# Optimization experiments

Hardware: AMD Instinct MI355X
Metric: run time of the kernel (lower is better)

The kernel has to match this reference:

```python
import jax, jax.numpy as jnp
import numpy as np

B, N, E = 2, 2048, 2048
H, G, D = 16, 4, 128          # num_heads, num_kv_groups, head_dim = E // H
HID = 4 * E                    # GeGLU hidden width
EPS = 1e-6


def setup_inputs() -> dict:
    key = jax.random.key(0)
    ks = jax.random.split(key, 8)
    g = lambda k, shape: jax.random.normal(k, shape, jnp.float32) * 0.02
    return {
        "x": jax.random.normal(ks[0], (B, N, E), jnp.float32),
        "wq": g(ks[1], (E, H * D)),
        "wk": g(ks[2], (E, G * D)),
        "wv": g(ks[3], (E, G * D)),
        "wo": g(ks[4], (H * D, E)),
        "w1": g(ks[5], (E, 2 * HID)),   # GeGLU in-proj (value | gate)
        "w2": g(ks[6], (HID, E)),       # GeGLU out-proj
        "norm1_w": jnp.ones((E,), jnp.float32),
        "norm2_w": jnp.ones((E,), jnp.float32),
    }


def _rope_cos_sin(n, d, dtype):
    inv_freq = 1.0 / (10000.0 ** (jnp.arange(0, d, 2, dtype=jnp.float32) / d))
    freqs = jnp.arange(n, dtype=jnp.float32)[:, None] * inv_freq[None, :]  # [n, d/2]
    emb = jnp.concatenate([freqs, freqs], axis=-1)                          # [n, d]
    return jnp.cos(emb).astype(dtype), jnp.sin(emb).astype(dtype)


def _rotate_half(t):
    d2 = t.shape[-1] // 2
    return jnp.concatenate([-t[..., d2:], t[..., :d2]], axis=-1)


def _apply_rope(t, cos, sin):
    # t: [b, h, n, d]; cos/sin: [n, d]
    return t * cos + _rotate_half(t) * sin


def _rmsnorm(x, w):
    var = jnp.mean(jnp.square(x), axis=-1, keepdims=True)
    return x * jax.lax.rsqrt(var + EPS) * w


def reference(x, wq, wk, wv, wo, w1, w2, norm1_w, norm2_w):
    b, n, _ = x.shape
    # q = k = v = x reshaped into heads (pre-projection, as in source)
    qkv = x.reshape(b, n, H, D).transpose(0, 2, 1, 3)  # [b, H, n, D]
    cos, sin = _rope_cos_sin(n, D, x.dtype)
    q_r = _apply_rope(qkv, cos, sin)
    k_r = _apply_rope(qkv, cos, sin)
    # flatten back to [b, n, E]
    q_flat = q_r.transpose(0, 2, 1, 3).reshape(b, n, E)
    k_flat = k_r.transpose(0, 2, 1, 3).reshape(b, n, E)
    v_flat = x  # v untouched by RoPE; flatten == x

    # Grouped-query attention with internal projections
    qh = (q_flat @ wq).reshape(b, n, H, D).transpose(0, 2, 1, 3)       # [b, H, n, D]
    kh = (k_flat @ wk).reshape(b, n, G, D)                              # [b, n, G, D]
    vh = (v_flat @ wv).reshape(b, n, G, D)
    kh = jnp.repeat(kh, H // G, axis=2).transpose(0, 2, 1, 3)           # [b, H, n, D]
    vh = jnp.repeat(vh, H // G, axis=2).transpose(0, 2, 1, 3)

    scale = 1.0 / np.sqrt(D)
    scores = jnp.einsum('bhqd,bhkd->bhqk', qh, kh) * scale
    attn = jax.nn.softmax(scores, axis=-1)                               # [b, H, n, n]
    ctx = jnp.einsum('bhqk,bhkd->bhqd', attn, vh)
    attn_out = ctx.transpose(0, 2, 1, 3).reshape(b, n, H * D) @ wo      # [b, n, E]

    x1 = _rmsnorm(x + attn_out, norm1_w)

    # GeGLU FFN
    uv = x1 @ w1
    u, gate = jnp.split(uv, 2, axis=-1)
    fc = (u * jax.nn.gelu(gate)) @ w2

    x2 = _rmsnorm(x1 + fc, norm2_w)
    return (x2, (k_flat, v_flat), attn)
```

## Files before the change

### kernel.cpp

```cpp
#include <hip/hip_runtime.h>
#include <hip/hip_bf16.h>


using f32x4  = __attribute__((ext_vector_type(4))) float;
using bf16x8 = __attribute__((ext_vector_type(8))) short;
using bf16x4 = __attribute__((ext_vector_type(4))) short;
using u16x4  = __attribute__((ext_vector_type(4))) unsigned short;

#define DEV __device__ __forceinline__

#define ASYNC16(lds, g)                                                        \
  __builtin_amdgcn_global_load_lds(                                           \
      (const __attribute__((address_space(1))) void*)(g),                      \
      (__attribute__((address_space(3))) void*)(lds), 16, 0, 0)

DEV unsigned short f2bf(float f) {
  unsigned int u = __float_as_uint(f);
  return (unsigned short)((u + 0x7fffu + ((u >> 16) & 1u)) >> 16);
}
DEV float bf2f(unsigned short h) {
  return __uint_as_float(((unsigned int)h) << 16);
}

DEV float waveRedSum(float v) {
#pragma unroll
  for (int o = 32; o; o >>= 1) v += __shfl_xor(v, o);
  return v;
}

__global__ __launch_bounds__(256) void kconvT(const float* __restrict__ in,
                                              unsigned short* __restrict__ out,
                                              int K, int N) {
  __shared__ float tile[32][33];
  int bx = blockIdx.x * 32;
  int by = blockIdx.y * 32;
  int tx = threadIdx.x & 31;
  int ty = threadIdx.x >> 5;
#pragma unroll
  for (int i = 0; i < 32; i += 8)
    tile[ty + i][tx] = in[(size_t)(by + ty + i) * N + bx + tx];
  __syncthreads();
#pragma unroll
  for (int i = 0; i < 32; i += 8)
    out[(size_t)(bx + ty + i) * K + by + tx] = f2bf(tile[tx][ty + i]);
}

__global__ __launch_bounds__(256) void krope(const float* __restrict__ x,
                                             float* __restrict__ kout,
                                             float* __restrict__ vout,
                                             unsigned short* __restrict__ xq,
                                             unsigned short* __restrict__ xb) {
  int idx = blockIdx.x * 256 + threadIdx.x;
  int f  = idx & 63;
  int h  = (idx >> 6) & 15;
  int bn = idx >> 10;
  int n  = bn & 2047;
  size_t base = (size_t)bn * 2048 + h * 128;
  float inv = exp2f((float)f * (-13.287712379549449f / 64.0f));
  float ang = (float)n * inv;
  float c = cosf(ang), s = sinf(ang);
  float a = x[base + f], b = x[base + f + 64];
  float k1 = a * c - b * s;
  float k2 = b * c + a * s;
  __builtin_nontemporal_store(k1, kout + base + f);
  __builtin_nontemporal_store(k2, kout + base + f + 64);
  xq[base + f]      = f2bf(k1);
  xq[base + f + 64] = f2bf(k2);
  __builtin_nontemporal_store(a, vout + base + f);
  __builtin_nontemporal_store(b, vout + base + f + 64);
  xb[base + f]      = f2bf(a);
  xb[base + f + 64] = f2bf(b);
}

__global__ __launch_bounds__(256) void krms1(const float* __restrict__ x,
                                             const float* __restrict__ ao,
                                             const float* __restrict__ w,
                                             unsigned short* __restrict__ x1b) {
  size_t row = blockIdx.x;
  const f32x4* xp = (const f32x4*)(x + row * 2048);
  const f32x4* ap = (const f32x4*)(ao + row * 2048);
  int tid = threadIdx.x;
  f32x4 t0 = xp[tid * 2] + ap[tid * 2];
  f32x4 t1 = xp[tid * 2 + 1] + ap[tid * 2 + 1];
  float ss = 0.f;
#pragma unroll
  for (int i = 0; i < 4; ++i) ss += t0[i] * t0[i] + t1[i] * t1[i];
  ss = waveRedSum(ss);
  __shared__ float red[4];
  int wid = tid >> 6, lane = tid & 63;
  if (!lane) red[wid] = ss;
  __syncthreads();
  ss = red[0] + red[1] + red[2] + red[3];
  float rr = rsqrtf(ss * (1.0f / 2048.0f) + 1e-6f);
  const f32x4* wp = (const f32x4*)w;
  f32x4 w0 = wp[tid * 2], w1 = wp[tid * 2 + 1];
  u16x4 o0, o1;
#pragma unroll
  for (int i = 0; i < 4; ++i) {
    o0[i] = f2bf(t0[i] * rr * w0[i]);
    o1[i] = f2bf(t1[i] * rr * w1[i]);
  }
  u16x4* op = (u16x4*)(x1b + row * 2048);
  op[tid * 2] = o0;
  op[tid * 2 + 1] = o1;
}

__global__ __launch_bounds__(256) void krms2(const unsigned short* __restrict__ x1b,
                                             const unsigned short* __restrict__ fc,
                                             const float* __restrict__ w,
                                             float* __restrict__ out) {
  size_t row = blockIdx.x;
  const u16x4* xp = (const u16x4*)(x1b + row * 2048);
  const u16x4* fp = (const u16x4*)(fc + row * 2048);
  int tid = threadIdx.x;
  u16x4 a0 = xp[tid * 2], a1 = xp[tid * 2 + 1];
  u16x4 b0 = fp[tid * 2], b1 = fp[tid * 2 + 1];
  f32x4 t0, t1;
#pragma unroll
  for (int i = 0; i < 4; ++i) {
    t0[i] = bf2f(a0[i]) + bf2f(b0[i]);
    t1[i] = bf2f(a1[i]) + bf2f(b1[i]);
  }
  float ss = 0.f;
#pragma unroll
  for (int i = 0; i < 4; ++i) ss += t0[i] * t0[i] + t1[i] * t1[i];
  ss = waveRedSum(ss);
  __shared__ float red[4];
  int wid = tid >> 6, lane = tid & 63;
  if (!lane) red[wid] = ss;
  __syncthreads();
  ss = red[0] + red[1] + red[2] + red[3];
  float rr = rsqrtf(ss * (1.0f / 2048.0f) + 1e-6f);
  const f32x4* wp = (const f32x4*)w;
  f32x4 w0 = wp[tid * 2], w1 = wp[tid * 2 + 1];
  f32x4* op = (f32x4*)(out + row * 2048);
  f32x4 o0 = t0 * rr * w0;
  f32x4 o1 = t1 * rr * w1;
  __builtin_nontemporal_store(o0, op + tid * 2);
  __builtin_nontemporal_store(o1, op + tid * 2 + 1);
}

template <bool OUT_BF16, bool TRANS_OUT>
__global__ __launch_bounds__(256, 2) void gemm_bt(
    const unsigned short* __restrict__ A, const unsigned short* __restrict__ Bt,
    void* __restrict__ C_, int K, int lda, int ldb, int ldc, float alpha) {
  __shared__ unsigned short As[128 * 32];
  __shared__ unsigned short Bs[128 * 32];
  const int tid = threadIdx.x;
  const int bm0 = blockIdx.y * 128, bn0 = blockIdx.x * 128;

  f32x4 acc[4][4] = {};

  const int lane = tid & 63, wid = tid >> 6;
  const int wr = wid >> 1, wc = wid & 1;
  const int lr = lane & 15, kq = lane >> 4;
  const int srow = tid >> 2;
  const int scol = (tid & 3) * 8;
  unsigned short* AsW = As + tid * 8;
  unsigned short* BsW = Bs + tid * 8;

  for (int kt = 0; kt < K; kt += 32) {
    ASYNC16(AsW,        A + (size_t)(bm0 + srow)      * lda + kt + scol);
    ASYNC16(AsW + 2048, A + (size_t)(bm0 + srow + 64) * lda + kt + scol);
    ASYNC16(BsW,        Bt + (size_t)(bn0 + srow)      * ldb + kt + scol);
    ASYNC16(BsW + 2048, Bt + (size_t)(bn0 + srow + 64) * ldb + kt + scol);
    __syncthreads();
    bf16x8 afr[4], bfr[4];
#pragma unroll
    for (int i = 0; i < 4; ++i)
      afr[i] = *(const bf16x8*)&As[(wr * 64 + i * 16 + lr) * 32 + kq * 8];
#pragma unroll
    for (int j = 0; j < 4; ++j)
      bfr[j] = *(const bf16x8*)&Bs[(wc * 64 + j * 16 + lr) * 32 + kq * 8];
#pragma unroll
    for (int i = 0; i < 4; ++i)
#pragma unroll
      for (int j = 0; j < 4; ++j)
        acc[i][j] = __builtin_amdgcn_mfma_f32_16x16x32_bf16(afr[i], bfr[j],
                                                            acc[i][j], 0, 0, 0);
    __syncthreads();
  }

#pragma unroll
  for (int i = 0; i < 4; ++i)
#pragma unroll
    for (int j = 0; j < 4; ++j) {
      int rowb = bm0 + wr * 64 + i * 16 + kq * 4;
      int col = bn0 + wc * 64 + j * 16 + lr;
#pragma unroll
      for (int r = 0; r < 4; ++r) {
        float v = acc[i][j][r] * alpha;
        size_t idx = TRANS_OUT ? ((size_t)col * ldc + (rowb + r))
                               : ((size_t)(rowb + r) * ldc + col);
        if constexpr (OUT_BF16)
          ((unsigned short*)C_)[idx] = f2bf(v);
        else
          ((float*)C_)[idx] = v;
      }
    }
}

__global__ __launch_bounds__(512, 4) void kattn(
    const unsigned short* __restrict__ qh,
    const unsigned short* __restrict__ kh,
    const unsigned short* __restrict__ vT,
    float* __restrict__ attn,
    unsigned short* __restrict__ ctx) {
  __shared__ __align__(16) char U[65536];
  __shared__ __align__(16) char Vb[16384];
  float* redm = (float*)Vb;
  float* reds = redm + 128;

  const int tid = threadIdx.x;
  const int lane = tid & 63, w = tid >> 6;
  const int lr = lane & 15, kq = lane >> 4;
  const int bid = blockIdx.x;
  const int g8 = bid & 7;
  const int j  = bid >> 3;
  const int bz = g8 >> 2;
  const int gz = g8 & 3;
  const int hz = gz * 4 + (j & 3);
  const int q0 = (j >> 2) << 4;
  const int z  = bz * 16 + hz;

  const unsigned short* Aq =
      qh + ((size_t)(bz * 2048 + q0 + lr) * 2048 + hz * 128);
  bf16x8 qfr[4];
#pragma unroll
  for (int kk = 0; kk < 4; ++kk)
    qfr[kk] = *(const bf16x8*)(Aq + kk * 32 + kq * 8);

  const unsigned short* Kb =
      kh + ((size_t)(bz * 2048) * 512 + gz * 128);
  int krow[4], kcs[4];
#pragma unroll
  for (int R = 0; R < 4; ++R) {
    int idx = R * 64 + lane;
    krow[R] = idx >> 4;
    kcs[R] = (idx & 15) ^ (krow[R] & 7);
  }
  auto stageK = [&](int buf, int t) {
#pragma unroll
    for (int R = 0; R < 4; ++R)
      ASYNC16(U + buf * 32768 + w * 4096 + (R * 64 + lane) * 16,
              Kb + (size_t)(t * 128 + w * 16 + krow[R]) * 512 + kcs[R] * 8);
  };

  f32x4 acc[16];
#pragma unroll
  for (int t = 0; t < 16; ++t) acc[t] = f32x4{0.f, 0.f, 0.f, 0.f};

  stageK(0, 0);
  stageK(1, 1);
#pragma unroll
  for (int t = 0; t < 16; ++t) {
    if (t < 15) asm volatile("s_waitcnt vmcnt(4)" ::: "memory");
    else        asm volatile("s_waitcnt vmcnt(0)" ::: "memory");
    __builtin_amdgcn_sched_barrier(0);
    const char* Kw = U + (t & 1) * 32768 + w * 4096;
    bf16x8 kfr[4];
#pragma unroll
    for (int kk = 0; kk < 4; ++kk) {
      int cch = (kk * 4 + kq) ^ (lr & 7);
      kfr[kk] = *(const bf16x8*)(Kw + lr * 256 + cch * 16);
    }
    asm volatile("s_waitcnt lgkmcnt(0)" ::: "memory");
    __builtin_amdgcn_sched_barrier(0);
    if (t + 2 < 16) stageK(t & 1, t + 2);
#pragma unroll
    for (int kk = 0; kk < 4; ++kk)
      acc[t] = __builtin_amdgcn_mfma_f32_16x16x32_bf16(kfr[kk], qfr[kk],
                                                       acc[t], 0, 0, 0);
  }

  const float scale = 0.08838834764831845f;
  float mx = -3.4e38f;
#pragma unroll
  for (int t = 0; t < 16; ++t) {
    acc[t] *= scale;
#pragma unroll
    for (int r = 0; r < 4; ++r) mx = fmaxf(mx, acc[t][r]);
  }
  mx = fmaxf(mx, __shfl_xor(mx, 16));
  mx = fmaxf(mx, __shfl_xor(mx, 32));
  if (kq == 0) redm[w * 16 + lr] = mx;
  __syncthreads();
  mx = redm[lr];
#pragma unroll
  for (int ww = 1; ww < 8; ++ww) mx = fmaxf(mx, redm[ww * 16 + lr]);

  float sm = 0.f;
#pragma unroll
  for (int t = 0; t < 16; ++t) {
#pragma unroll
    for (int r = 0; r < 4; ++r) {
      float e = __expf(acc[t][r] - mx);
      acc[t][r] = e;
      sm += e;
    }
  }
  sm += __shfl_xor(sm, 16);
  sm += __shfl_xor(sm, 32);
  if (kq == 0) reds[w * 16 + lr] = sm;
  __syncthreads();
  float smt = reds[lr];
#pragma unroll
  for (int ww = 1; ww < 8; ++ww) smt += reds[ww * 16 + lr];
  float inv = 1.0f / smt;

  float* arow = attn + (((size_t)z * 2048 + q0 + lr) * 2048);
#pragma unroll
  for (int t = 0; t < 16; ++t) {
    int key = t * 128 + w * 16 + kq * 4;
    f32x4 p = acc[t] * inv;
    __builtin_nontemporal_store(p, (f32x4*)(arow + key));
    bf16x4 pb;
#pragma unroll
    for (int r = 0; r < 4; ++r) pb[r] = (short)f2bf(p[r]);
    int c8 = key >> 3;
    *(bf16x4*)(U + lr * 4096 + ((c8 ^ (lr & 7)) << 4) + ((key & 7) << 1)) = pb;
  }
  __syncthreads();

  const unsigned short* Bv = vT + (size_t)gz * 524288 + bz * 2048;
  const int d0 = w * 16;
  const int vd = lane >> 2;
  const int vcs = (lane & 3) ^ (vd & 3);
  auto stageV = [&](int buf, int t) {
    ASYNC16(Vb + buf * 8192 + w * 1024 + lane * 16,
            Bv + (size_t)(d0 + vd) * 4096 + t * 32 + vcs * 8);
  };

  f32x4 cfr = {};
  stageV(0, 0);
  stageV(1, 1);
#pragma unroll
  for (int t = 0; t < 64; ++t) {
    if (t < 63) asm volatile("s_waitcnt vmcnt(1)" ::: "memory");
    else        asm volatile("s_waitcnt vmcnt(0)" ::: "memory");
    __builtin_amdgcn_sched_barrier(0);
    int c8 = t * 4 + kq;
    bf16x8 pfr = *(const bf16x8*)(U + lr * 4096 + ((c8 ^ (lr & 7)) << 4));
    const char* Vw = Vb + (t & 1) * 8192 + w * 1024;
    bf16x8 vfr = *(const bf16x8*)(Vw + lr * 64 + ((kq ^ (lr & 3)) << 4));
    asm volatile("s_waitcnt lgkmcnt(0)" ::: "memory");
    __builtin_amdgcn_sched_barrier(0);
    if (t + 2 < 64) stageV(t & 1, t + 2);
    cfr = __builtin_amdgcn_mfma_f32_16x16x32_bf16(pfr, vfr, cfr, 0, 0, 0);
  }
#pragma unroll
  for (int r = 0; r < 4; ++r) {
    int q = kq * 4 + r;
    ctx[((size_t)(bz * 2048 + q0 + q) * 2048) + hz * 128 + d0 + lr] =
        f2bf(cfr[r]);
  }
}

template <bool OUT_BF16>
__global__ __launch_bounds__(512, 2) void gemm128(
    const unsigned short* __restrict__ A, const unsigned short* __restrict__ Bt,
    void* __restrict__ C_, int K, int lda, int ldb, int ldc) {
  __shared__ unsigned short As[2][128 * 64];
  __shared__ unsigned short Bs[2][128 * 64];
  const int tid = threadIdx.x;
  const int bm0 = blockIdx.y * 128, bn0 = blockIdx.x * 128;
  const int lane = tid & 63, wid = tid >> 6;
  const int wr = wid >> 2, wc = wid & 3;
  const int lr = lane & 15, kq = lane >> 4;

  f32x4 acc[4][2] = {};

  int sArow[2], sAcc[2];
#pragma unroll
  for (int R = 0; R < 2; ++R) {
    int c = R * 512 + tid;
    sArow[R] = c >> 3;
    sAcc[R]  = (c & 7) ^ (sArow[R] & 7);
  }

  auto stage = [&](int buf, int k0) {
#pragma unroll
    for (int R = 0; R < 2; ++R)
      ASYNC16(&As[buf][(R * 512 + tid) * 8],
              A + (size_t)(bm0 + sArow[R]) * lda + k0 + sAcc[R] * 8);
#pragma unroll
    for (int R = 0; R < 2; ++R)
      ASYNC16(&Bs[buf][(R * 512 + tid) * 8],
              Bt + (size_t)(bn0 + sArow[R]) * ldb + k0 + sAcc[R] * 8);
  };

  const int NT = K >> 6;
  stage(0, 0);
  stage(1, 64);
  int cur = 0;
  for (int t = 0; t < NT; ++t) {
    if (t + 1 < NT) asm volatile("s_waitcnt vmcnt(4)" ::: "memory");
    else            asm volatile("s_waitcnt vmcnt(0)" ::: "memory");
    __builtin_amdgcn_sched_barrier(0);
    __builtin_amdgcn_s_barrier();
    __builtin_amdgcn_sched_barrier(0);
    const unsigned short* Ac = As[cur];
    const unsigned short* Bc = Bs[cur];
    bf16x8 afr0[4], bfr0[2];
#pragma unroll
    for (int i = 0; i < 4; ++i) {
      int row = wr * 64 + i * 16 + lr;
      afr0[i] = *(const bf16x8*)&Ac[(row * 8 + (kq ^ (row & 7))) * 8];
    }
#pragma unroll
    for (int j2 = 0; j2 < 2; ++j2) {
      int brow = wc * 32 + j2 * 16 + lr;
      bfr0[j2] = *(const bf16x8*)&Bc[(brow * 8 + (kq ^ (brow & 7))) * 8];
    }
    __builtin_amdgcn_s_setprio(1);
#pragma unroll
    for (int j2 = 0; j2 < 2; ++j2)
#pragma unroll
      for (int i = 0; i < 4; ++i)
        acc[i][j2] = __builtin_amdgcn_mfma_f32_16x16x32_bf16(afr0[i], bfr0[j2],
                                                             acc[i][j2], 0, 0, 0);
    __builtin_amdgcn_s_setprio(0);
    bf16x8 afr1[4], bfr1[2];
#pragma unroll
    for (int i = 0; i < 4; ++i) {
      int row = wr * 64 + i * 16 + lr;
      afr1[i] = *(const bf16x8*)&Ac[(row * 8 + ((4 + kq) ^ (row & 7))) * 8];
    }
#pragma unroll
    for (int j2 = 0; j2 < 2; ++j2) {
      int brow = wc * 32 + j2 * 16 + lr;
      bfr1[j2] = *(const bf16x8*)&Bc[(brow * 8 + ((4 + kq) ^ (brow & 7))) * 8];
    }
    asm volatile("s_waitcnt lgkmcnt(0)" ::: "memory");
    __builtin_amdgcn_sched_barrier(0);
    __builtin_amdgcn_s_barrier();
    __builtin_amdgcn_sched_barrier(0);
    if (t + 2 < NT) stage(cur, (t + 2) << 6);
    __builtin_amdgcn_s_setprio(1);
#pragma unroll
    for (int j2 = 0; j2 < 2; ++j2)
#pragma unroll
      for (int i = 0; i < 4; ++i)
        acc[i][j2] = __builtin_amdgcn_mfma_f32_16x16x32_bf16(afr1[i], bfr1[j2],
                                                             acc[i][j2], 0, 0, 0);
    __builtin_amdgcn_s_setprio(0);
    cur ^= 1;
  }

#pragma unroll
  for (int i = 0; i < 4; ++i)
#pragma unroll
    for (int j = 0; j < 2; ++j) {
      int rowb = bm0 + wr * 64 + i * 16 + kq * 4;
      int col = bn0 + wc * 32 + j * 16 + lr;
#pragma unroll
      for (int r = 0; r < 4; ++r) {
        if constexpr (OUT_BF16)
          ((unsigned short*)C_)[(size_t)(rowb + r) * ldc + col] = f2bf(acc[i][j][r]);
        else
          ((float*)C_)[(size_t)(rowb + r) * ldc + col] = acc[i][j][r];
      }
    }
}

__global__ __launch_bounds__(512, 2) void gemm_geglu256(
    const unsigned short* __restrict__ A, const unsigned short* __restrict__ B1,
    const unsigned short* __restrict__ B2, unsigned short* __restrict__ H_,
    int K, int lda, int ldb, int ldc) {
  __shared__ unsigned short As[2][256 * 64];
  __shared__ unsigned short B1s[2][128 * 64];
  __shared__ unsigned short B2s[2][128 * 64];
  const int tid = threadIdx.x;
  const int bm0 = blockIdx.y * 256, bn0 = blockIdx.x * 128;
  const int lane = tid & 63, wid = tid >> 6;
  const int wr = wid >> 2, wc = wid & 3;
  const int lr = lane & 15, kq = lane >> 4;

  f32x4 accu[8][2] = {};
  f32x4 accg[8][2] = {};

  int sArow[4], sAcc[4], sBrow[2], sBcc[2];
#pragma unroll
  for (int R = 0; R < 4; ++R) {
    int c = R * 512 + tid;
    sArow[R] = c >> 3;
    sAcc[R]  = (c & 7) ^ (sArow[R] & 7);
  }
#pragma unroll
  for (int R = 0; R < 2; ++R) {
    int c = R * 512 + tid;
    sBrow[R] = c >> 3;
    sBcc[R]  = (c & 7) ^ (sBrow[R] & 7);
  }

  auto stage = [&](int buf, int k0) {
#pragma unroll
    for (int R = 0; R < 4; ++R)
      ASYNC16(&As[buf][(R * 512 + tid) * 8],
              A + (size_t)(bm0 + sArow[R]) * lda + k0 + sAcc[R] * 8);
#pragma unroll
    for (int R = 0; R < 2; ++R)
      ASYNC16(&B1s[buf][(R * 512 + tid) * 8],
              B1 + (size_t)(bn0 + sBrow[R]) * ldb + k0 + sBcc[R] * 8);
#pragma unroll
    for (int R = 0; R < 2; ++R)
      ASYNC16(&B2s[buf][(R * 512 + tid) * 8],
              B2 + (size_t)(bn0 + sBrow[R]) * ldb + k0 + sBcc[R] * 8);
  };

  const int NT = K >> 6;
  stage(0, 0);
  stage(1, 64);
  int cur = 0;
  for (int t = 0; t < NT; ++t) {
    if (t + 1 < NT) asm volatile("s_waitcnt vmcnt(8)" ::: "memory");
    else            asm volatile("s_waitcnt vmcnt(0)" ::: "memory");
    __builtin_amdgcn_sched_barrier(0);
    __builtin_amdgcn_s_barrier();
    __builtin_amdgcn_sched_barrier(0);
    const unsigned short* Ac = As[cur];
    const unsigned short* B1c = B1s[cur];
    const unsigned short* B2c = B2s[cur];
    bf16x8 afr0[8], b10[2], b20[2];
#pragma unroll
    for (int i = 0; i < 8; ++i) {
      int row = wr * 128 + i * 16 + lr;
      afr0[i] = *(const bf16x8*)&Ac[(row * 8 + (kq ^ (row & 7))) * 8];
    }
#pragma unroll
    for (int j2 = 0; j2 < 2; ++j2) {
      int brow = wc * 32 + j2 * 16 + lr;
      b10[j2] = *(const bf16x8*)&B1c[(brow * 8 + (kq ^ (brow & 7))) * 8];
      b20[j2] = *(const bf16x8*)&B2c[(brow * 8 + (kq ^ (brow & 7))) * 8];
    }
    __builtin_amdgcn_s_setprio(1);
#pragma unroll
    for (int j2 = 0; j2 < 2; ++j2)
#pragma unroll
      for (int i = 0; i < 8; ++i) {
        accu[i][j2] = __builtin_amdgcn_mfma_f32_16x16x32_bf16(afr0[i], b10[j2],
                                                              accu[i][j2], 0, 0, 0);
        accg[i][j2] = __builtin_amdgcn_mfma_f32_16x16x32_bf16(afr0[i], b20[j2],
                                                              accg[i][j2], 0, 0, 0);
      }
    __builtin_amdgcn_s_setprio(0);
    bf16x8 afr1[8], b11[2], b21[2];
#pragma unroll
    for (int i = 0; i < 8; ++i) {
      int row = wr * 128 + i * 16 + lr;
      afr1[i] = *(const bf16x8*)&Ac[(row * 8 + ((4 + kq) ^ (row & 7))) * 8];
    }
#pragma unroll
    for (int j2 = 0; j2 < 2; ++j2) {
      int brow = wc * 32 + j2 * 16 + lr;
      b11[j2] = *(const bf16x8*)&B1c[(brow * 8 + ((4 + kq) ^ (brow & 7))) * 8];
      b21[j2] = *(const bf16x8*)&B2c[(brow * 8 + ((4 + kq) ^ (brow & 7))) * 8];
    }
    asm volatile("s_waitcnt lgkmcnt(0)" ::: "memory");
    __builtin_amdgcn_sched_barrier(0);
    __builtin_amdgcn_s_barrier();
    __builtin_amdgcn_sched_barrier(0);
    if (t + 2 < NT) stage(cur, (t + 2) << 6);
    __builtin_amdgcn_s_setprio(1);
#pragma unroll
    for (int j2 = 0; j2 < 2; ++j2)
#pragma unroll
      for (int i = 0; i < 8; ++i) {
        accu[i][j2] = __builtin_amdgcn_mfma_f32_16x16x32_bf16(afr1[i], b11[j2],
                                                              accu[i][j2], 0, 0, 0);
        accg[i][j2] = __builtin_amdgcn_mfma_f32_16x16x32_bf16(afr1[i], b21[j2],
                                                              accg[i][j2], 0, 0, 0);
      }
    __builtin_amdgcn_s_setprio(0);
    cur ^= 1;
  }

#pragma unroll
  for (int i = 0; i < 8; ++i)
#pragma unroll
    for (int j = 0; j < 2; ++j) {
      int rowb = bm0 + wr * 128 + i * 16 + kq * 4;
      int col = bn0 + wc * 32 + j * 16 + lr;
#pragma unroll
      for (int r = 0; r < 4; ++r) {
        float u = accu[i][j][r];
        float g = accg[i][j][r];
        float tv = tanhf(0.7978845608028654f * (g + 0.044715f * g * g * g));
        float hv = u * 0.5f * g * (1.0f + tv);
        H_[(size_t)(rowb + r) * ldc + col] = f2bf(hv);
      }
    }
}

extern "C" void kernel_launch(void* const* d_in, const int* in_sizes, int n_in,
                              void* d_out, int out_size, void* d_ws, size_t ws_size,
                              hipStream_t stream) {
  const float* x   = (const float*)d_in[0];
  const float* wq  = (const float*)d_in[1];
  const float* wk  = (const float*)d_in[2];
  const float* wv  = (const float*)d_in[3];
  const float* wo  = (const float*)d_in[4];
  const float* w1  = (const float*)d_in[5];
  const float* w2  = (const float*)d_in[6];
  const float* n1w = (const float*)d_in[7];
  const float* n2w = (const float*)d_in[8];

  float* out    = (float*)d_out;
  float* x2_out = out;
  float* k_out  = out + 8388608;
  float* v_out  = out + 16777216;
  float* attn   = out + 25165824;

  char* ws = (char*)d_ws;
  unsigned short* wqT  = (unsigned short*)(ws + 0);
  unsigned short* wkT  = (unsigned short*)(ws + 8388608);
  unsigned short* wvT  = (unsigned short*)(ws + 10485760);
  unsigned short* woT  = (unsigned short*)(ws + 12582912);
  unsigned short* w1T  = (unsigned short*)(ws + 20971520);
  unsigned short* w2T  = (unsigned short*)(ws + 88080384);
  unsigned short* qh   = (unsigned short*)(ws + 121634816);
  unsigned short* kh   = (unsigned short*)(ws + 138412032);
  unsigned short* vhT  = (unsigned short*)(ws + 142606336);
  unsigned short* ctx  = (unsigned short*)(ws + 146800640);
  float*          ao   = (float*)(ws + 163577856);
  unsigned short* hbuf = (unsigned short*)(ws + 121634816);
  unsigned short* x1b  = (unsigned short*)(ws + 197132288);
  unsigned short* fc   = (unsigned short*)(ws + 213909504);

  unsigned short* xb = (unsigned short*)attn;
  unsigned short* xq = xb + 8388608;

  dim3 blk(256);
  dim3 blk512(512);

  kconvT<<<dim3(64, 64), blk, 0, stream>>>(wq, wqT, 2048, 2048);
  kconvT<<<dim3(16, 64), blk, 0, stream>>>(wk, wkT, 2048, 512);
  kconvT<<<dim3(16, 64), blk, 0, stream>>>(wv, wvT, 2048, 512);
  kconvT<<<dim3(64, 64), blk, 0, stream>>>(wo, woT, 2048, 2048);
  kconvT<<<dim3(512, 64), blk, 0, stream>>>(w1, w1T, 2048, 16384);
  kconvT<<<dim3(64, 256), blk, 0, stream>>>(w2, w2T, 8192, 2048);

  krope<<<16384, blk, 0, stream>>>(x, k_out, v_out, xq, xb);

  gemm128<true><<<dim3(16, 32), blk512, 0, stream>>>(
      xq, wqT, qh, 2048, 2048, 2048, 2048);
  gemm_bt<true, false><<<dim3(4, 32), blk, 0, stream>>>(
      xq, wkT, kh, 2048, 2048, 2048, 512, 1.0f);
  gemm_bt<true, true><<<dim3(4, 32), blk, 0, stream>>>(
      xb, wvT, vhT, 2048, 2048, 2048, 4096, 1.0f);

  kattn<<<dim3(4096), blk512, 0, stream>>>(qh, kh, vhT, attn, ctx);

  gemm128<false><<<dim3(16, 32), blk512, 0, stream>>>(
      ctx, woT, (void*)ao, 2048, 2048, 2048, 2048);
  krms1<<<4096, blk, 0, stream>>>(x, ao, n1w, x1b);
  gemm_geglu256<<<dim3(64, 16), blk512, 0, stream>>>(
      x1b, w1T, w1T + 16777216, hbuf, 2048, 2048, 2048, 8192);
  gemm128<true><<<dim3(16, 32), blk512, 0, stream>>>(
      hbuf, w2T, fc, 8192, 8192, 8192, 2048);
  krms2<<<4096, blk, 0, stream>>>(x1b, fc, n2w, x2_out);
}
```

Baseline: 940.7 us.

## Merge weight conversions and K/V projections into single launches, raise MFMA priority

Folds the five fp32-to-bf16 transposes for wq/wk/wv/wo/w1 into one kernel that picks its source matrix from the block column, which relies on the destination buffers being laid out back to back. Merges the K and V projection GEMMs into one launch, using blockIdx.z to choose operands and output layout, so 256 blocks share a single launch. Wraps the MFMA loops in the attention kernel with s_setprio to favour the issuing wave. The aim is fewer kernel launches and better fill of small grids; the combined conversion only works if the workspace offsets stay contiguous.

```diff
diff --git a/kernel.cpp b/kernel.cpp
--- a/kernel.cpp
+++ b/kernel.cpp
@@ -26,6 +26,30 @@
 #pragma unroll
   for (int o = 32; o; o >>= 1) v += __shfl_xor(v, o);
   return v;
+}
+
+__global__ __launch_bounds__(256) void kconvAll(
+    const float* __restrict__ wq, const float* __restrict__ wk,
+    const float* __restrict__ wv, const float* __restrict__ wo,
+    const float* __restrict__ w1, unsigned short* __restrict__ dst) {
+  __shared__ float tile[32][33];
+  int bx = blockIdx.x * 32;
+  int by = blockIdx.y * 32;
+  const float* src; int nsrc, c0;
+  if (bx < 2048)      { src = wq; nsrc = 2048;  c0 = bx; }
+  else if (bx < 2560) { src = wk; nsrc = 512;   c0 = bx - 2048; }
+  else if (bx < 3072) { src = wv; nsrc = 512;   c0 = bx - 2560; }
+  else if (bx < 5120) { src = wo; nsrc = 2048;  c0 = bx - 3072; }
+  else                { src = w1; nsrc = 16384; c0 = bx - 5120; }
+  int tx = threadIdx.x & 31;
+  int ty = threadIdx.x >> 5;
+#pragma unroll
+  for (int i = 0; i < 32; i += 8)
+    tile[ty + i][tx] = src[(size_t)(by + ty + i) * nsrc + c0 + tx];
+  __syncthreads();
+#pragma unroll
+  for (int i = 0; i < 32; i += 8)
+    dst[(size_t)(bx + ty + i) * 2048 + by + tx] = f2bf(tile[tx][ty + i]);
 }
 
 __global__ __launch_bounds__(256) void kconvT(const float* __restrict__ in,
@@ -140,10 +164,13 @@
   __builtin_nontemporal_store(o1, op + tid * 2 + 1);
 }
 
-template <bool OUT_BF16, bool TRANS_OUT>
-__global__ __launch_bounds__(256, 2) void gemm_bt(
-    const unsigned short* __restrict__ A, const unsigned short* __restrict__ Bt,
-    void* __restrict__ C_, int K, int lda, int ldb, int ldc, float alpha) {
+__global__ __launch_bounds__(256, 2) void kvproj(
+    const unsigned short* __restrict__ xq, const unsigned short* __restrict__ xb,
+    const unsigned short* __restrict__ wkT, const unsigned short* __restrict__ wvT,
+    unsigned short* __restrict__ kh, unsigned short* __restrict__ vhT) {
+  const bool isV = blockIdx.z != 0;
+  const unsigned short* A  = isV ? xb : xq;
+  const unsigned short* Bt = isV ? wvT : wkT;
   __shared__ unsigned short As[128 * 32];
   __shared__ unsigned short Bs[128 * 32];
   const int tid = threadIdx.x;
@@ -159,11 +186,11 @@
   unsigned short* AsW = As + tid * 8;
   unsigned short* BsW = Bs + tid * 8;
 
-  for (int kt = 0; kt < K; kt += 32) {
-    ASYNC16(AsW,        A + (size_t)(bm0 + srow)      * lda + kt + scol);
-    ASYNC16(AsW + 2048, A + (size_t)(bm0 + srow + 64) * lda + kt + scol);
-    ASYNC16(BsW,        Bt + (size_t)(bn0 + srow)      * ldb + kt + scol);
-    ASYNC16(BsW + 2048, Bt + (size_t)(bn0 + srow + 64) * ldb + kt + scol);
+  for (int kt = 0; kt < 2048; kt += 32) {
+    ASYNC16(AsW,        A + (size_t)(bm0 + srow)      * 2048 + kt + scol);
+    ASYNC16(AsW + 2048, A + (size_t)(bm0 + srow + 64) * 2048 + kt + scol);
+    ASYNC16(BsW,        Bt + (size_t)(bn0 + srow)      * 2048 + kt + scol);
+    ASYNC16(BsW + 2048, Bt + (size_t)(bn0 + srow + 64) * 2048 + kt + scol);
     __syncthreads();
     bf16x8 afr[4], bfr[4];
 #pragma unroll
@@ -189,13 +216,9 @@
       int col = bn0 + wc * 64 + j * 16 + lr;
 #pragma unroll
       for (int r = 0; r < 4; ++r) {
-        float v = acc[i][j][r] * alpha;
-        size_t idx = TRANS_OUT ? ((size_t)col * ldc + (rowb + r))
-                               : ((size_t)(rowb + r) * ldc + col);
-        if constexpr (OUT_BF16)
-          ((unsigned short*)C_)[idx] = f2bf(v);
-        else
-          ((float*)C_)[idx] = v;
+        unsigned short v = f2bf(acc[i][j][r]);
+        if (isV) vhT[(size_t)col * 4096 + (rowb + r)] = v;
+        else     kh[(size_t)(rowb + r) * 512 + col] = v;
       }
     }
 }
@@ -267,10 +290,12 @@
     asm volatile("s_waitcnt lgkmcnt(0)" ::: "memory");
     __builtin_amdgcn_sched_barrier(0);
     if (t + 2 < 16) stageK(t & 1, t + 2);
+    __builtin_amdgcn_s_setprio(1);
 #pragma unroll
     for (int kk = 0; kk < 4; ++kk)
       acc[t] = __builtin_amdgcn_mfma_f32_16x16x32_bf16(kfr[kk], qfr[kk],
                                                        acc[t], 0, 0, 0);
+    __builtin_amdgcn_s_setprio(0);
   }
 
   const float scale = 0.08838834764831845f;
@@ -346,7 +371,9 @@
     asm volatile("s_waitcnt lgkmcnt(0)" ::: "memory");
     __builtin_amdgcn_sched_barrier(0);
     if (t + 2 < 64) stageV(t & 1, t + 2);
+    __builtin_amdgcn_s_setprio(1);
     cfr = __builtin_amdgcn_mfma_f32_16x16x32_bf16(pfr, vfr, cfr, 0, 0, 0);
+    __builtin_amdgcn_s_setprio(0);
   }
 #pragma unroll
   for (int r = 0; r < 4; ++r) {
@@ -633,21 +660,14 @@
   dim3 blk(256);
   dim3 blk512(512);
 
-  kconvT<<<dim3(64, 64), blk, 0, stream>>>(wq, wqT, 2048, 2048);
-  kconvT<<<dim3(16, 64), blk, 0, stream>>>(wk, wkT, 2048, 512);
-  kconvT<<<dim3(16, 64), blk, 0, stream>>>(wv, wvT, 2048, 512);
-  kconvT<<<dim3(64, 64), blk, 0, stream>>>(wo, woT, 2048, 2048);
-  kconvT<<<dim3(512, 64), blk, 0, stream>>>(w1, w1T, 2048, 16384);
+  kconvAll<<<dim3(672, 64), blk, 0, stream>>>(wq, wk, wv, wo, w1, wqT);
   kconvT<<<dim3(64, 256), blk, 0, stream>>>(w2, w2T, 8192, 2048);
 
   krope<<<16384, blk, 0, stream>>>(x, k_out, v_out, xq, xb);
 
   gemm128<true><<<dim3(16, 32), blk512, 0, stream>>>(
       xq, wqT, qh, 2048, 2048, 2048, 2048);
-  gemm_bt<true, false><<<dim3(4, 32), blk, 0, stream>>>(
-      xq, wkT, kh, 2048, 2048, 2048, 512, 1.0f);
-  gemm_bt<true, true><<<dim3(4, 32), blk, 0, stream>>>(
-      xb, wvT, vhT, 2048, 2048, 2048, 4096, 1.0f);
+  kvproj<<<dim3(4, 32, 2), blk, 0, stream>>>(xq, xb, wkT, wvT, kh, vhT);
 
   kattn<<<dim3(4096), blk512, 0, stream>>>(qh, kh, vhT, attn, ctx);
 
```

Measured after the change: 915.2 us. 2.7% less time.
